# Optimization experiments

Hardware: AMD Instinct MI355X
Metric: run time of the kernel (lower is better)

Reference implementation:

```python
import jax, jax.numpy as jnp
import numpy as np

SR = 32000
N_FFT = 1024
HOP = 320
N_MELS = 128
PCEN_S = 0.025
PCEN_ALPHA = 0.98
PCEN_DELTA = 2.0
PCEN_R = 0.5
EPS = 1e-06


def _mel_filterbank():
    # torchaudio melscale_fbanks defaults: HTK mel scale, norm=None, f_min=0, f_max=sr/2
    n_freqs = N_FFT // 2 + 1
    all_freqs = np.linspace(0.0, SR / 2.0, n_freqs)
    def hz_to_mel(f):
        return 2595.0 * np.log10(1.0 + f / 700.0)
    def mel_to_hz(m):
        return 700.0 * (10.0 ** (m / 2595.0) - 1.0)
    m_pts = np.linspace(hz_to_mel(0.0), hz_to_mel(SR / 2.0), N_MELS + 2)
    f_pts = mel_to_hz(m_pts)
    f_diff = f_pts[1:] - f_pts[:-1]                      # (n_mels+1,)
    slopes = f_pts[None, :] - all_freqs[:, None]          # (n_freqs, n_mels+2)
    down = -slopes[:, :-2] / f_diff[:-1]
    up = slopes[:, 2:] / f_diff[1:]
    fb = np.maximum(0.0, np.minimum(down, up))            # (n_freqs, n_mels)
    return jnp.asarray(fb, dtype=jnp.float32)


def _mel_spectrogram(x):
    # x: [B, 1, L]; torch.stft semantics: center=True, reflect pad, periodic hann, power=1
    pad = N_FFT // 2
    xp = jnp.pad(x, ((0, 0), (0, 0), (pad, pad)), mode='reflect')
    L = xp.shape[-1]
    n_frames = 1 + (L - N_FFT) // HOP                      # 401
    idx = jnp.arange(n_frames)[:, None] * HOP + jnp.arange(N_FFT)[None, :]
    frames = xp[..., idx]                                  # [B, 1, T, n_fft]
    n = jnp.arange(N_FFT, dtype=jnp.float32)
    window = 0.5 * (1.0 - jnp.cos(2.0 * jnp.pi * n / N_FFT))  # periodic hann
    spec = jnp.abs(jnp.fft.rfft(frames * window, axis=-1))    # [B, 1, T, F]
    fb = _mel_filterbank()                                    # [F, n_mels]
    mel = jnp.einsum('bctf,fm->bcmt', spec, fb)               # [B, 1, n_mels, T]
    return mel


def _pcen_iir(mel, s):
    # first-order recurrence M_t = (1-s) M_{t-1} + s x_t, M_0 = x_0, along last axis
    xt = jnp.moveaxis(mel, -1, 0)                          # [T, B, 1, M]
    def step(carry, x_t):
        m = (1.0 - s) * carry + s * x_t
        return m, m
    _, rest = jax.lax.scan(step, xt[0], xt[1:])
    M = jnp.concatenate([xt[:1], rest], axis=0)
    return jnp.moveaxis(M, 0, -1)


def setup_inputs() -> dict:
    key = jax.random.key(0)
    x = jax.random.normal(key, (128, 1, 128000), dtype=jnp.float32)
    return {"x": x}


def reference(x):
    mel = _mel_spectrogram(x)                              # [B,1,128,401]
    mel_smooth = _pcen_iir(mel, PCEN_S)
    smooth = jnp.power(EPS + mel_smooth, PCEN_ALPHA)
    pcen = jnp.power(mel / smooth + PCEN_DELTA, PCEN_R) - PCEN_DELTA ** PCEN_R
    mean = jnp.mean(pcen, axis=(2, 3), keepdims=True)
    std = jnp.std(pcen, axis=(2, 3), keepdims=True, ddof=1)  # torch std is unbiased
    return (pcen - mean) / (std + 1e-06)
```

## Files before the change

### kernel.cpp

```cpp
#include <hip/hip_runtime.h>
#include <math.h>

#define SR        32000
#define NFFT      1024
#define HOP       320
#define NMELS     128
#define NFREQS    513
#define LIN       128000
#define PADL      512
#define TFRAMES   401
#define NB        128

#define WS_WIN    0
#define WS_FBT    1024
#define WS_FS     66816
#define WS_FE     66944
#define WS_PART   67072
#define WS_MEL    69120
#define FBSTRIDE  514

__global__ void prep_kernel(float* __restrict__ win, float* __restrict__ fbT,
                            int* __restrict__ fstart, int* __restrict__ fend) {
    const int tid = threadIdx.x;

    for (int i = tid; i < NFFT; i += 256) {
        float ang = (float)i * (float)(2.0 * M_PI / (double)NFFT);
        win[i] = 0.5f - 0.5f * cosf(ang);
    }

    if (tid < NMELS) {
        const int m = tid;
        const double mel_max = 2595.0 * log10(1.0 + ((double)SR * 0.5) / 700.0);
        const double m0 = (double)(m)     * mel_max / (double)(NMELS + 1);
        const double m1 = (double)(m + 1) * mel_max / (double)(NMELS + 1);
        const double m2 = (double)(m + 2) * mel_max / (double)(NMELS + 1);
        const double f0 = 700.0 * (pow(10.0, m0 / 2595.0) - 1.0);
        const double f1 = 700.0 * (pow(10.0, m1 / 2595.0) - 1.0);
        const double f2 = 700.0 * (pow(10.0, m2 / 2595.0) - 1.0);
        const double binw = (double)SR * 0.5 / (double)(NFREQS - 1);
        int fs = (int)(f0 / binw) + 1;
        int fe = (int)ceil(f2 / binw);
        fs = (fs > 0) ? fs - 1 : 0;
        fe = (fe < NFREQS) ? fe + 1 : NFREQS;
        for (int f = fs; f < fe; ++f) {
            double freq = (double)f * binw;
            double down = (freq - f0) / (f1 - f0);
            double up   = (f2 - freq) / (f2 - f1);
            double v = fmin(down, up);
            v = fmax(0.0, v);
            fbT[m * FBSTRIDE + f] = (float)v;
        }
        fstart[m] = fs;
        fend[m]   = fe;
    }
}

__device__ __forceinline__ void dft16(float (&xr)[16], float (&xi)[16]) {
    const float C8 = 0.92387953251128674f;
    const float S8 = 0.38268343236508978f;
    const float R2 = 0.70710678118654752f;
    const float WR[4][4] = {{1,1,1,1},{1, C8, R2, S8},{1, R2, 0.f,-R2},{1, S8,-R2,-C8}};
    const float WI[4][4] = {{0,0,0,0},{0,-S8,-R2,-C8},{0,-R2,-1.f,-R2},{0,-C8,-R2, S8}};
    float pr[4][4], pi[4][4];
#pragma unroll
    for (int j0 = 0; j0 < 4; ++j0) {
        float ar = xr[j0],      ai = xi[j0];
        float br = xr[j0 + 4],  bi = xi[j0 + 4];
        float cr = xr[j0 + 8],  ci = xi[j0 + 8];
        float dr = xr[j0 + 12], di = xi[j0 + 12];
        float t0r = ar + cr, t0i = ai + ci;
        float t1r = ar - cr, t1i = ai - ci;
        float t2r = br + dr, t2i = bi + di;
        float t3r = br - dr, t3i = bi - di;
        pr[j0][0] = t0r + t2r; pi[j0][0] = t0i + t2i;
        pr[j0][1] = t1r + t3i; pi[j0][1] = t1i - t3r;
        pr[j0][2] = t0r - t2r; pi[j0][2] = t0i - t2i;
        pr[j0][3] = t1r - t3i; pi[j0][3] = t1i + t3r;
    }
#pragma unroll
    for (int ka = 0; ka < 4; ++ka) {
        float q0r = pr[0][ka], q0i = pi[0][ka];
        float q1r = pr[1][ka] * WR[1][ka] - pi[1][ka] * WI[1][ka];
        float q1i = pr[1][ka] * WI[1][ka] + pi[1][ka] * WR[1][ka];
        float q2r = pr[2][ka] * WR[2][ka] - pi[2][ka] * WI[2][ka];
        float q2i = pr[2][ka] * WI[2][ka] + pi[2][ka] * WR[2][ka];
        float q3r = pr[3][ka] * WR[3][ka] - pi[3][ka] * WI[3][ka];
        float q3i = pr[3][ka] * WI[3][ka] + pi[3][ka] * WR[3][ka];
        float t0r = q0r + q2r, t0i = q0i + q2i;
        float t1r = q0r - q2r, t1i = q0i - q2i;
        float t2r = q1r + q3r, t2i = q1i + q3i;
        float t3r = q1r - q3r, t3i = q1i - q3i;
        xr[ka]      = t0r + t2r; xi[ka]      = t0i + t2i;
        xr[ka + 4]  = t1r + t3i; xi[ka + 4]  = t1i - t3r;
        xr[ka + 8]  = t0r - t2r; xi[ka + 8]  = t0i - t2i;
        xr[ka + 12] = t1r - t3i; xi[ka + 12] = t1i + t3r;
    }
}

__launch_bounds__(256)
__global__ void fft_mel_kernel(const float* __restrict__ x,
                               const float* __restrict__ win,
                               const float* __restrict__ fbT,
                               const int* __restrict__ fstart,
                               const int* __restrict__ fend,
                               float* __restrict__ mel) {
    __shared__ __align__(16) float2 buf[4][NFFT];
    __shared__ float2 magb[4][514];

    const int w = threadIdx.x >> 6;
    const int t = threadIdx.x & 63;
    const int task = blockIdx.x * 4 + w;
    const int q  = task / TFRAMES;
    const int tf = task - q * TFRAMES;
    const float* xb0 = x + (size_t)(2 * q) * LIN;
    const float* xb1 = xb0 + LIN;
    const int base = tf * HOP - PADL;

    float xr[16], xi[16];
#pragma unroll
    for (int j = 0; j < 16; ++j) {
        int n = t + 64 * j;
        int p = base + n;
        p = (p < 0) ? -p : p;
        p = (p >= LIN) ? (2 * LIN - 2 - p) : p;
        float wv = win[n];
        xr[j] = xb0[p] * wv;
        xi[j] = xb1[p] * wv;
    }

    dft16(xr, xi);
    {
        float sw, cw;
        sincosf((float)t * -6.135923151542565e-3f, &sw, &cw);
        float ur = 1.0f, ui = 0.0f;
#pragma unroll
        for (int k1 = 1; k1 < 16; ++k1) {
            float nr = ur * cw - ui * sw;
            ui = ur * sw + ui * cw;
            ur = nr;
            float tr = xr[k1] * ur - xi[k1] * ui;
            xi[k1] = xr[k1] * ui + xi[k1] * ur;
            xr[k1] = tr;
        }
    }

    float2* B = buf[w];
#pragma unroll
    for (int k1 = 0; k1 < 16; ++k1)
        B[k1 * 64 + (t ^ ((k1 & 3) << 2))] = make_float2(xr[k1], xi[k1]);

    const int g = t >> 2, s = t & 3;
    const int c2 = g & 3;
#pragma unroll
    for (int j = 0; j < 16; ++j) {
        float2 v = B[g * 64 + s + 4 * (j ^ c2)];
        xr[j] = v.x; xi[j] = v.y;
    }

    dft16(xr, xi);
    {
        float sw, cw;
        sincosf((float)s * -9.817477042468103e-2f, &sw, &cw);
        float ur = 1.0f, ui = 0.0f;
#pragma unroll
        for (int k2 = 1; k2 < 16; ++k2) {
            float nr = ur * cw - ui * sw;
            ui = ur * sw + ui * cw;
            ur = nr;
            float tr = xr[k2] * ur - xi[k2] * ui;
            xi[k2] = xr[k2] * ui + xi[k2] * ur;
            xr[k2] = tr;
        }
    }

    {
        const int g2 = (g & 7) << 1;
#pragma unroll
        for (int k2 = 0; k2 < 16; ++k2)
            B[g * 64 + ((4 * k2 + s) ^ g2)] = make_float2(xr[k2], xi[k2]);
    }

    const float4* Bv = (const float4*)buf[w];
    const int gk = t & 15;
    const int g2k = (gk & 7) << 1;
    const int tb = t >> 4;
#pragma unroll
    for (int jj = 0; jj < 8; ++jj) {
        const int k  = t + 64 * jj;
        const int jk = (tb + 4 * jj) & 15;
        const int e0 = gk * 64 + ((4 * jk) ^ g2k);
        float4 E01 = Bv[e0 >> 1];
        float4 E23 = Bv[(e0 ^ 2) >> 1];
        float S02r = E01.x + E23.x, S02i = E01.y + E23.y;
        float D02r = E01.x - E23.x, D02i = E01.y - E23.y;
        float S13r = E01.z + E23.z, S13i = E01.w + E23.w;
        float D13r = E01.z - E23.z, D13i = E01.w - E23.w;
        float a, b;
        if (jj < 4) { a = S02r + S13r; b = S02i + S13i; }
        else        { a = D02r + D13i; b = D02i - D13r; }
        const int kN = (1024 - k) & 1023;
        const int gN = kN & 15, jN = (kN >> 4) & 15, bN = kN >> 8;
        const int eN = gN * 64 + ((4 * jN) ^ ((gN & 7) << 1));
        float4 F01 = Bv[eN >> 1];
        float4 F23 = Bv[(eN ^ 2) >> 1];
        float GS02r = F01.x + F23.x, GS02i = F01.y + F23.y;
        float GD02r = F01.x - F23.x, GD02i = F01.y - F23.y;
        float GS13r = F01.z + F23.z, GS13i = F01.w + F23.w;
        float GD13r = F01.z - F23.z, GD13i = F01.w - F23.w;
        const float sE = (bN & 2) ? -1.0f : 1.0f;
        float cEv = GS02r + sE * GS13r, dEv = GS02i + sE * GS13i;
        float cOv = GD02r + sE * GD13i, dOv = GD02i - sE * GD13r;
        float c = (bN & 1) ? cOv : cEv;
        float d = (bN & 1) ? dOv : dEv;
        float m0 = 0.5f * sqrtf((a + c) * (a + c) + (b - d) * (b - d));
        float m1 = 0.5f * sqrtf((b + d) * (b + d) + (c - a) * (c - a));
        magb[w][k] = make_float2(m0, m1);
    }
    if (t == 0) {
        float4 E01 = Bv[0], E23 = Bv[1];
        float a = (E01.x + E23.x) - (E01.z + E23.z);
        float b = (E01.y + E23.y) - (E01.w + E23.w);
        magb[w][512] = make_float2(fabsf(a), fabsf(b));
    }

#pragma unroll
    for (int h = 0; h < 2; ++h) {
        const int m = t + 64 * h;
        const int fs = fstart[m], fe = fend[m];
        const float* fr = fbT + m * FBSTRIDE;
        float a0 = 0.0f, a1 = 0.0f;
        for (int f = fs; f < fe; ++f) {
            float2 mg = magb[w][f];
            float cf = fr[f];
            a0 = fmaf(mg.x, cf, a0);
            a1 = fmaf(mg.y, cf, a1);
        }
        mel[((size_t)(2 * q)     * TFRAMES + tf) * NMELS + m] = a0;
        mel[((size_t)(2 * q + 1) * TFRAMES + tf) * NMELS + m] = a1;
    }
}

#define CHUNKS 8
#define CH0LEN 51
#define CHLEN  50
#define AFACT  0.28202481f

__launch_bounds__(256)
__global__ void pcen_kernel(const float* __restrict__ mel,
                            float* __restrict__ out,
                            double* __restrict__ partials) {
    const int b   = blockIdx.x >> 2;
    const int mg  = blockIdx.x & 3;
    const int tid = threadIdx.x;
    const int ml  = tid & 31;
    const int c   = tid >> 5;
    const int m   = mg * 32 + ml;
    const int t0  = (c == 0) ? 0 : (CH0LEN + CHLEN * (c - 1));
    const int len = (c == 0) ? CH0LEN : CHLEN;
    const float* mb = mel + (size_t)b * TFRAMES * NMELS;

    float v[CH0LEN];
#pragma unroll
    for (int i = 0; i < CH0LEN; ++i)
        if (i < len) v[i] = mb[(size_t)(t0 + i) * NMELS + m];

    float M;
    if (c == 0) {
        M = v[0];
#pragma unroll
        for (int i = 1; i < CH0LEN; ++i) M = fmaf(0.975f, M, 0.025f * v[i]);
    } else {
        M = 0.0f;
#pragma unroll
        for (int i = 0; i < CHLEN; ++i) M = fmaf(0.975f, M, 0.025f * v[i]);
    }
    __shared__ float Bc[CHUNKS][32];
    Bc[c][ml] = M;
    __syncthreads();

    float Min = 0.0f;
    if (c > 0) {
        Min = Bc[0][ml];
        for (int k = 1; k < c; ++k) Min = fmaf(AFACT, Min, Bc[k][ml]);
    }

    M = Min;
    float sum = 0.0f, sumsq = 0.0f;
    float* orow = out + (size_t)b * NMELS * TFRAMES + (size_t)m * TFRAMES + t0;
#pragma unroll
    for (int i = 0; i < CH0LEN; ++i) {
        if (i < len) {
            float xt = v[i];
            M = (c == 0 && i == 0) ? xt : fmaf(0.975f, M, 0.025f * xt);
            float smooth = __expf(0.98f * __logf(1e-6f + M));
            float p = sqrtf(xt / smooth + 2.0f) - 1.4142135623730951f;
            orow[i] = p;
            sum += p;
            sumsq = fmaf(p, p, sumsq);
        }
    }

    double s = (double)sum, qq = (double)sumsq;
    for (int off = 32; off > 0; off >>= 1) {
        s  += __shfl_down(s, off);
        qq += __shfl_down(qq, off);
    }
    __shared__ double wsum[4], wsq[4];
    const int wid = tid >> 6, lane = tid & 63;
    if (lane == 0) { wsum[wid] = s; wsq[wid] = qq; }
    __syncthreads();
    if (tid == 0) {
        double S = wsum[0] + wsum[1] + wsum[2] + wsum[3];
        double Q = wsq[0] + wsq[1] + wsq[2] + wsq[3];
        partials[(size_t)(b * 4 + mg) * 2]     = S;
        partials[(size_t)(b * 4 + mg) * 2 + 1] = Q;
    }
}

__global__ void norm_kernel(float* __restrict__ out, const double* __restrict__ partials) {
    __shared__ float sh[2];
    const int b = blockIdx.x;
    if (threadIdx.x == 0) {
        double S = 0.0, Q = 0.0;
#pragma unroll
        for (int gg = 0; gg < 4; ++gg) {
            S += partials[(size_t)(b * 4 + gg) * 2];
            Q += partials[(size_t)(b * 4 + gg) * 2 + 1];
        }
        const double n = (double)(NMELS * TFRAMES);
        double mean = S / n;
        double var  = (Q - n * mean * mean) / (n - 1.0);
        double sd   = sqrt(var > 0.0 ? var : 0.0);
        sh[0] = (float)mean;
        sh[1] = (float)(1.0 / (sd + 1e-6));
    }
    __syncthreads();
    const int i4 = blockIdx.y * 256 + threadIdx.x;
    if (i4 >= NMELS * TFRAMES / 4) return;
    const float mean = sh[0], inv = sh[1];
    float4* o = (float4*)(out + (size_t)b * NMELS * TFRAMES);
    float4 vv = o[i4];
    vv.x = (vv.x - mean) * inv;
    vv.y = (vv.y - mean) * inv;
    vv.z = (vv.z - mean) * inv;
    vv.w = (vv.w - mean) * inv;
    o[i4] = vv;
}

extern "C" void kernel_launch(void* const* d_in, const int* in_sizes, int n_in,
                              void* d_out, int out_size, void* d_ws, size_t ws_size,
                              hipStream_t stream) {
    const float* x = (const float*)d_in[0];
    float* out = (float*)d_out;
    float* ws  = (float*)d_ws;

    float*  win    = ws + WS_WIN;
    float*  fbT    = ws + WS_FBT;
    int*    fstart = (int*)(ws + WS_FS);
    int*    fend   = (int*)(ws + WS_FE);
    double* parts  = (double*)(ws + WS_PART);
    float*  mel    = ws + WS_MEL;

    prep_kernel<<<dim3(1), dim3(256), 0, stream>>>(win, fbT, fstart, fend);
    fft_mel_kernel<<<dim3((NB / 2) * TFRAMES / 4), dim3(256), 0, stream>>>(
        x, win, fbT, fstart, fend, mel);
    pcen_kernel<<<dim3(NB * 4), dim3(256), 0, stream>>>(mel, out, parts);
    norm_kernel<<<dim3(NB, 51), dim3(256), 0, stream>>>(out, parts);
}
```

Measured before the change: 206.0 us.

## Precompute FFT twiddle tables, add interior fast path, vectorize PCEN scan

Twiddle factors are precomputed in double precision into global tables by the prep kernel, and the FFT stages read them in place of running a sincos plus a recurrence per thread. The frame-load path skips the reflect-index arithmetic for frames fully inside the signal. The PCEN kernel is restructured to have each thread process four mel bins as float4 over 16 time chunks, re-reading mel from global instead of caching 51 values in registers. This halves the block count and changes the chunk-carry factor. The aim is to cut ALU work in the FFT and improve load vectorization in PCEN, at the cost of extra global reads and fewer blocks.

```diff
diff --git a/kernel.cpp b/kernel.cpp
--- a/kernel.cpp
+++ b/kernel.cpp
@@ -15,17 +15,31 @@
 #define WS_FBT    1024
 #define WS_FS     66816
 #define WS_FE     66944
-#define WS_PART   67072
-#define WS_MEL    69120
+#define WS_T1     67072
+#define WS_T2     69120
+#define WS_PART   69248
+#define WS_MEL    70272
 #define FBSTRIDE  514
 
 __global__ void prep_kernel(float* __restrict__ win, float* __restrict__ fbT,
-                            int* __restrict__ fstart, int* __restrict__ fend) {
+                            int* __restrict__ fstart, int* __restrict__ fend,
+                            float2* __restrict__ T1, float2* __restrict__ T2) {
     const int tid = threadIdx.x;
 
     for (int i = tid; i < NFFT; i += 256) {
-        float ang = (float)i * (float)(2.0 * M_PI / (double)NFFT);
-        win[i] = 0.5f - 0.5f * cosf(ang);
+        double ang = 2.0 * M_PI * (double)i / (double)NFFT;
+        win[i] = (float)(0.5 - 0.5 * cos(ang));
+    }
+
+    for (int idx = tid; idx < 1024; idx += 256) {
+        int tt = idx >> 4, k1 = idx & 15;
+        double ang = -2.0 * M_PI * (double)(tt * k1) / 1024.0;
+        T1[idx] = make_float2((float)cos(ang), (float)sin(ang));
+    }
+    if (tid < 64) {
+        int s = tid >> 4, k2 = tid & 15;
+        double ang = -2.0 * M_PI * (double)(s * k2) / 64.0;
+        T2[tid] = make_float2((float)cos(ang), (float)sin(ang));
     }
 
     if (tid < NMELS) {
@@ -100,6 +114,8 @@
 __launch_bounds__(256)
 __global__ void fft_mel_kernel(const float* __restrict__ x,
                                const float* __restrict__ win,
+                               const float2* __restrict__ T1,
+                               const float2* __restrict__ T2,
                                const float* __restrict__ fbT,
                                const int* __restrict__ fstart,
                                const int* __restrict__ fend,
@@ -117,29 +133,35 @@
     const int base = tf * HOP - PADL;
 
     float xr[16], xi[16];
-#pragma unroll
-    for (int j = 0; j < 16; ++j) {
-        int n = t + 64 * j;
-        int p = base + n;
-        p = (p < 0) ? -p : p;
-        p = (p >= LIN) ? (2 * LIN - 2 - p) : p;
-        float wv = win[n];
-        xr[j] = xb0[p] * wv;
-        xi[j] = xb1[p] * wv;
+    if (base >= 0 && base + NFFT <= LIN) {
+#pragma unroll
+        for (int j = 0; j < 16; ++j) {
+            int n = t + 64 * j;
+            float wv = win[n];
+            xr[j] = xb0[base + n] * wv;
+            xi[j] = xb1[base + n] * wv;
+        }
+    } else {
+#pragma unroll
+        for (int j = 0; j < 16; ++j) {
+            int n = t + 64 * j;
+            int p = base + n;
+            p = (p < 0) ? -p : p;
+            p = (p >= LIN) ? (2 * LIN - 2 - p) : p;
+            float wv = win[n];
+            xr[j] = xb0[p] * wv;
+            xi[j] = xb1[p] * wv;
+        }
     }
 
     dft16(xr, xi);
     {
-        float sw, cw;
-        sincosf((float)t * -6.135923151542565e-3f, &sw, &cw);
-        float ur = 1.0f, ui = 0.0f;
+        const float2* __restrict__ Tr = T1 + (t << 4);
 #pragma unroll
         for (int k1 = 1; k1 < 16; ++k1) {
-            float nr = ur * cw - ui * sw;
-            ui = ur * sw + ui * cw;
-            ur = nr;
-            float tr = xr[k1] * ur - xi[k1] * ui;
-            xi[k1] = xr[k1] * ui + xi[k1] * ur;
+            const float2 wv = Tr[k1];
+            const float tr = xr[k1] * wv.x - xi[k1] * wv.y;
+            xi[k1] = xr[k1] * wv.y + xi[k1] * wv.x;
             xr[k1] = tr;
         }
     }
@@ -159,16 +181,12 @@
 
     dft16(xr, xi);
     {
-        float sw, cw;
-        sincosf((float)s * -9.817477042468103e-2f, &sw, &cw);
-        float ur = 1.0f, ui = 0.0f;
+        const float2* __restrict__ Tr = T2 + (s << 4);
 #pragma unroll
         for (int k2 = 1; k2 < 16; ++k2) {
-            float nr = ur * cw - ui * sw;
-            ui = ur * sw + ui * cw;
-            ur = nr;
-            float tr = xr[k2] * ur - xi[k2] * ui;
-            xi[k2] = xr[k2] * ui + xi[k2] * ur;
+            const float2 wv = Tr[k2];
+            const float tr = xr[k2] * wv.x - xi[k2] * wv.y;
+            xi[k2] = xr[k2] * wv.y + xi[k2] * wv.x;
             xr[k2] = tr;
         }
     }
@@ -240,64 +258,85 @@
     }
 }
 
-#define CHUNKS 8
-#define CH0LEN 51
-#define CHLEN  50
-#define AFACT  0.28202481f
+#define CHUNKS 16
+#define CH0LEN 26
+#define CHLEN  25
+#define AFACT  0.53102595f
 
 __launch_bounds__(256)
 __global__ void pcen_kernel(const float* __restrict__ mel,
                             float* __restrict__ out,
                             double* __restrict__ partials) {
-    const int b   = blockIdx.x >> 2;
-    const int mg  = blockIdx.x & 3;
-    const int tid = threadIdx.x;
-    const int ml  = tid & 31;
-    const int c   = tid >> 5;
-    const int m   = mg * 32 + ml;
-    const int t0  = (c == 0) ? 0 : (CH0LEN + CHLEN * (c - 1));
-    const int len = (c == 0) ? CH0LEN : CHLEN;
-    const float* mb = mel + (size_t)b * TFRAMES * NMELS;
-
-    float v[CH0LEN];
-#pragma unroll
-    for (int i = 0; i < CH0LEN; ++i)
-        if (i < len) v[i] = mb[(size_t)(t0 + i) * NMELS + m];
-
-    float M;
+    const int b    = blockIdx.x >> 1;
+    const int half = blockIdx.x & 1;
+    const int tid  = threadIdx.x;
+    const int qd   = tid & 15;
+    const int c    = tid >> 4;
+    const int qg   = half * 16 + qd;
+    const int t0   = (c == 0) ? 0 : (CH0LEN + CHLEN * (c - 1));
+    const int len  = (c == 0) ? CH0LEN : CHLEN;
+    const float4* mb4 = (const float4*)(mel + (size_t)b * TFRAMES * NMELS);
+
+    float4 M4;
     if (c == 0) {
-        M = v[0];
-#pragma unroll
-        for (int i = 1; i < CH0LEN; ++i) M = fmaf(0.975f, M, 0.025f * v[i]);
+        M4 = mb4[qg];
+        for (int t = 1; t < CH0LEN; ++t) {
+            float4 xv = mb4[t * 32 + qg];
+            M4.x = fmaf(0.975f, M4.x, 0.025f * xv.x);
+            M4.y = fmaf(0.975f, M4.y, 0.025f * xv.y);
+            M4.z = fmaf(0.975f, M4.z, 0.025f * xv.z);
+            M4.w = fmaf(0.975f, M4.w, 0.025f * xv.w);
+        }
     } else {
-        M = 0.0f;
-#pragma unroll
-        for (int i = 0; i < CHLEN; ++i) M = fmaf(0.975f, M, 0.025f * v[i]);
-    }
-    __shared__ float Bc[CHUNKS][32];
-    Bc[c][ml] = M;
+        M4 = make_float4(0.f, 0.f, 0.f, 0.f);
+        for (int i = 0; i < CHLEN; ++i) {
+            float4 xv = mb4[(t0 + i) * 32 + qg];
+            M4.x = fmaf(0.975f, M4.x, 0.025f * xv.x);
+            M4.y = fmaf(0.975f, M4.y, 0.025f * xv.y);
+            M4.z = fmaf(0.975f, M4.z, 0.025f * xv.z);
+            M4.w = fmaf(0.975f, M4.w, 0.025f * xv.w);
+        }
+    }
+    __shared__ float4 Bc[CHUNKS][16];
+    Bc[c][qd] = M4;
     __syncthreads();
 
-    float Min = 0.0f;
+    float4 Min = make_float4(0.f, 0.f, 0.f, 0.f);
     if (c > 0) {
-        Min = Bc[0][ml];
-        for (int k = 1; k < c; ++k) Min = fmaf(AFACT, Min, Bc[k][ml]);
-    }
-
-    M = Min;
+        Min = Bc[0][qd];
+        for (int k = 1; k < c; ++k) {
+            float4 bv = Bc[k][qd];
+            Min.x = fmaf(AFACT, Min.x, bv.x);
+            Min.y = fmaf(AFACT, Min.y, bv.y);
+            Min.z = fmaf(AFACT, Min.z, bv.z);
+            Min.w = fmaf(AFACT, Min.w, bv.w);
+        }
+    }
+
+    float4 M = Min;
     float sum = 0.0f, sumsq = 0.0f;
-    float* orow = out + (size_t)b * NMELS * TFRAMES + (size_t)m * TFRAMES + t0;
-#pragma unroll
-    for (int i = 0; i < CH0LEN; ++i) {
-        if (i < len) {
-            float xt = v[i];
-            M = (c == 0 && i == 0) ? xt : fmaf(0.975f, M, 0.025f * xt);
-            float smooth = __expf(0.98f * __logf(1e-6f + M));
-            float p = sqrtf(xt / smooth + 2.0f) - 1.4142135623730951f;
-            orow[i] = p;
-            sum += p;
-            sumsq = fmaf(p, p, sumsq);
-        }
+    float* o0 = out + (size_t)b * NMELS * TFRAMES + (size_t)(qg * 4) * TFRAMES;
+    for (int i = 0; i < len; ++i) {
+        const int t = t0 + i;
+        float4 xv = mb4[t * 32 + qg];
+        if (c == 0 && i == 0) {
+            M = xv;
+        } else {
+            M.x = fmaf(0.975f, M.x, 0.025f * xv.x);
+            M.y = fmaf(0.975f, M.y, 0.025f * xv.y);
+            M.z = fmaf(0.975f, M.z, 0.025f * xv.z);
+            M.w = fmaf(0.975f, M.w, 0.025f * xv.w);
+        }
+        float p0 = sqrtf(xv.x / __expf(0.98f * __logf(1e-6f + M.x)) + 2.0f) - 1.4142135623730951f;
+        float p1 = sqrtf(xv.y / __expf(0.98f * __logf(1e-6f + M.y)) + 2.0f) - 1.4142135623730951f;
+        float p2 = sqrtf(xv.z / __expf(0.98f * __logf(1e-6f + M.z)) + 2.0f) - 1.4142135623730951f;
+        float p3 = sqrtf(xv.w / __expf(0.98f * __logf(1e-6f + M.w)) + 2.0f) - 1.4142135623730951f;
+        o0[t]               = p0;
+        o0[TFRAMES + t]     = p1;
+        o0[2 * TFRAMES + t] = p2;
+        o0[3 * TFRAMES + t] = p3;
+        sum += (p0 + p1) + (p2 + p3);
+        sumsq = fmaf(p0, p0, fmaf(p1, p1, fmaf(p2, p2, fmaf(p3, p3, sumsq))));
     }
 
     double s = (double)sum, qq = (double)sumsq;
@@ -312,8 +351,8 @@
     if (tid == 0) {
         double S = wsum[0] + wsum[1] + wsum[2] + wsum[3];
         double Q = wsq[0] + wsq[1] + wsq[2] + wsq[3];
-        partials[(size_t)(b * 4 + mg) * 2]     = S;
-        partials[(size_t)(b * 4 + mg) * 2 + 1] = Q;
+        partials[(size_t)(b * 2 + half) * 2]     = S;
+        partials[(size_t)(b * 2 + half) * 2 + 1] = Q;
     }
 }
 
@@ -323,9 +362,9 @@
     if (threadIdx.x == 0) {
         double S = 0.0, Q = 0.0;
 #pragma unroll
-        for (int gg = 0; gg < 4; ++gg) {
-            S += partials[(size_t)(b * 4 + gg) * 2];
-            Q += partials[(size_t)(b * 4 + gg) * 2 + 1];
+        for (int gg = 0; gg < 2; ++gg) {
+            S += partials[(size_t)(b * 2 + gg) * 2];
+            Q += partials[(size_t)(b * 2 + gg) * 2 + 1];
         }
         const double n = (double)(NMELS * TFRAMES);
         double mean = S / n;
@@ -358,12 +397,14 @@
     float*  fbT    = ws + WS_FBT;
     int*    fstart = (int*)(ws + WS_FS);
     int*    fend   = (int*)(ws + WS_FE);
+    float2* T1     = (float2*)(ws + WS_T1);
+    float2* T2     = (float2*)(ws + WS_T2);
     double* parts  = (double*)(ws + WS_PART);
     float*  mel    = ws + WS_MEL;
 
-    prep_kernel<<<dim3(1), dim3(256), 0, stream>>>(win, fbT, fstart, fend);
+    prep_kernel<<<dim3(1), dim3(256), 0, stream>>>(win, fbT, fstart, fend, T1, T2);
     fft_mel_kernel<<<dim3((NB / 2) * TFRAMES / 4), dim3(256), 0, stream>>>(
-        x, win, fbT, fstart, fend, mel);
-    pcen_kernel<<<dim3(NB * 4), dim3(256), 0, stream>>>(mel, out, parts);
+        x, win, T1, T2, fbT, fstart, fend, mel);
+    pcen_kernel<<<dim3(NB * 2), dim3(256), 0, stream>>>(mel, out, parts);
     norm_kernel<<<dim3(NB, 51), dim3(256), 0, stream>>>(out, parts);
 }
```

New measurement: 335.6 us. 62.9% more time.
